# Kernel optimization log

Hardware: AMD Instinct MI355X
Metric: run time of the kernel (lower is better)

The kernel has to match this reference:

```python
import jax, jax.numpy as jnp
import numpy as np

NEG_SLOPE = 0.01  # torch F.leaky_relu default
NUM_USER, NUM_ITEM, DIM = 50000, 30000, 64
N_NODES = NUM_USER + NUM_ITEM
N_INTER = 800000
N_LAYERS = 2


def _leaky(x):
    return jax.nn.leaky_relu(x, NEG_SLOPE)


def _gcn_tower(features, preference, id_embedding, W, b, row, col):
    # x = cat(preference, features); F.normalize (L2 per row)
    x = jnp.concatenate([preference, features], axis=0)  # [N, 64]
    x = x / jnp.maximum(jnp.linalg.norm(x, axis=1, keepdims=True), 1e-12)
    deg = jax.ops.segment_sum(jnp.ones(row.shape, x.dtype), row, num_segments=N_NODES)  # bincount(row)
    for i in range(N_LAYERS):
        # Abstract_GCN: scatter-mean of gathered neighbor feats, then linear
        agg = jax.ops.segment_sum(x[col], row, num_segments=N_NODES) / deg[:, None]
        h = _leaky(agg @ W[i, 0].T + b[i, 0])
        # has_id=True, concate=False
        x_hat = _leaky(x @ W[i, 1].T + b[i, 1]) + id_embedding
        x = _leaky(h @ W[i, 2].T + b[i, 2] + x_hat)
    return x


def setup_inputs() -> dict:
    key = jax.random.key(0)
    ks = jax.random.split(key, 14)
    # bipartite user->item edges with full node coverage (every node appears
    # as a row after symmetrization, matching real interaction data where
    # bincount(row) has no zeros)
    r1 = jnp.arange(NUM_USER, dtype=jnp.int64 if jax.config.jax_enable_x64 else jnp.int32)
    c1 = jax.random.randint(ks[0], (NUM_USER,), NUM_USER, N_NODES)
    r2 = jax.random.randint(ks[1], (NUM_ITEM,), 0, NUM_USER)
    c2 = NUM_USER + jnp.arange(NUM_ITEM, dtype=r1.dtype)
    rest = N_INTER - NUM_USER - NUM_ITEM
    r3 = jax.random.randint(ks[2], (rest,), 0, NUM_USER)
    c3 = jax.random.randint(ks[3], (rest,), NUM_USER, N_NODES)
    row0 = jnp.concatenate([r1, r2, r3])
    col0 = jnp.concatenate([c1, c2, c3])
    # symmetrize: cat(edge_index, edge_index[[1,0]])
    edge_index = jnp.stack([jnp.concatenate([row0, col0]),
                            jnp.concatenate([col0, row0])])  # [2, 1.6M]
    s = 0.1  # xavier-ish scale for 64x64
    return {
        "v_feat": jax.random.normal(ks[4], (NUM_ITEM, DIM), jnp.float32),
        "t_feat": jax.random.normal(ks[5], (NUM_ITEM, DIM), jnp.float32),
        "id_embedding": jax.random.normal(ks[6], (N_NODES, DIM), jnp.float32) * s,
        "v_pref": jax.random.normal(ks[7], (NUM_USER, DIM), jnp.float32) * s,
        "t_pref": jax.random.normal(ks[8], (NUM_USER, DIM), jnp.float32) * s,
        "v_W": jax.random.normal(ks[9], (N_LAYERS, 3, DIM, DIM), jnp.float32) * s,
        "v_b": jnp.zeros((N_LAYERS, 3, DIM), jnp.float32),
        "t_W": jax.random.normal(ks[10], (N_LAYERS, 3, DIM, DIM), jnp.float32) * s,
        "t_b": jnp.zeros((N_LAYERS, 3, DIM), jnp.float32),
        "edge_index": edge_index,
    }


def reference(v_feat, t_feat, id_embedding, v_pref, t_pref, v_W, v_b, t_W, t_b, edge_index):
    row, col = edge_index[0], edge_index[1]
    rep_v = _gcn_tower(v_feat, v_pref, id_embedding, v_W, v_b, row, col)
    rep_t = _gcn_tower(t_feat, t_pref, id_embedding, t_W, t_b, row, col)
    return (rep_v + rep_t) / 2.0  # MMGCN.get_rep representation
```

## Files before the change

kernel.cpp:

```cpp
#include <hip/hip_runtime.h>
#include <hip/hip_bf16.h>

#define NUM_USER 50000
#define N_NODES  80000
#define DIM      64
#define NEG_SLOPE 0.01f

#define NB 313
#define BSHIFT 8
#define RMASK 255
#define CSHIFT 17
#define CMASK 0x1FFFF

typedef __attribute__((ext_vector_type(8))) short short8;
typedef __attribute__((ext_vector_type(4))) float f32x4;

typedef unsigned short XT;

__device__ __forceinline__ float leaky(float v) {
    return v > 0.0f ? v : v * NEG_SLOPE;
}

__device__ __forceinline__ int load_idx(const void* ei, int is64, long long pos) {
    if (is64) return (int)((const long long*)ei)[pos];
    return ((const int*)ei)[pos];
}
__device__ __forceinline__ float load_f(const void* p, int isbf16, size_t i) {
    if (isbf16) return __bfloat162float(((const __hip_bfloat16*)p)[i]);
    return ((const float*)p)[i];
}

__device__ __forceinline__ unsigned short f2bf(float f) {
    unsigned u = __float_as_uint(f);
    u += 0x7fffu + ((u >> 16) & 1u);
    return (unsigned short)(u >> 16);
}

__global__ void detect_kernel(const unsigned int* __restrict__ feat_words,
                              const int* __restrict__ ei_words,
                              int* __restrict__ flags) {
    int lane = threadIdx.x & 63;
    int orv = 0;
    for (int i = lane * 2 + 1; i < 1024; i += 128) orv |= ei_words[i];
    int hits = 0;
    for (int i = lane; i < 256; i += 64) {
        unsigned e = (feat_words[i] >> 7) & 0xFF;
        hits += (e == 126 || e == 127) ? 1 : 0;
    }
    #pragma unroll
    for (int d = 32; d > 0; d >>= 1) {
        orv  |= __shfl_xor(orv, d, 64);
        hits += __shfl_xor(hits, d, 64);
    }
    if (lane == 0 && blockIdx.x == 0) {
        flags[0] = (orv == 0) ? 1 : 0;
        flags[1] = (hits > 64) ? 1 : 0;
    }
}

__global__ __launch_bounds__(1024) void prep_kernel(
        const void* __restrict__ vW, const void* __restrict__ tW,
        const void* __restrict__ vb, const void* __restrict__ tb,
        const int* __restrict__ flags,
        int* __restrict__ bucketCnt, unsigned short* __restrict__ Wbf,
        float* __restrict__ bfp) {
    int idx = blockIdx.x * blockDim.x + threadIdx.x;
    int isb = flags[1];
    if (idx < 320) {
        bucketCnt[idx] = 0;
    } else {
        int j = idx - 320;
        if (j < 2 * 24576) {
            int tw = j / 24576, r = j % 24576;
            Wbf[j] = f2bf(load_f(tw ? tW : vW, isb, r));
        } else if (j < 2 * 24576 + 2 * 384) {
            int i2 = j - 2 * 24576;
            int tw = i2 / 384, r = i2 % 384;
            bfp[i2] = load_f(tw ? tb : vb, isb, r);
        }
    }
}

__global__ __launch_bounds__(256) void countinit_kernel(
        const void* __restrict__ ei, int E, int cntBlocks,
        const int* __restrict__ flags,
        int* __restrict__ bucketCnt,
        const void* __restrict__ vp, const void* __restrict__ tp,
        const void* __restrict__ vf, const void* __restrict__ tf,
        XT* __restrict__ xc) {
    if ((int)blockIdx.x < cntBlocks) {
        __shared__ int bcnt[320];
        int tid = threadIdx.x;
        for (int i = tid; i < 320; i += 256) bcnt[i] = 0;
        __syncthreads();
        int is64 = flags[0];
        int base = blockIdx.x * 2048;
        #pragma unroll
        for (int it = 0; it < 8; ++it) {
            int e = base + it * 256 + tid;
            if (e < E) {
                int r = load_idx(ei, is64, e);
                int c = load_idx(ei, is64, (long long)E + e);
                if ((unsigned)r < N_NODES && (unsigned)c < N_NODES)
                    atomicAdd(&bcnt[r >> BSHIFT], 1);
            }
        }
        __syncthreads();
        for (int i = tid; i < NB; i += 256) {
            int v = bcnt[i];
            if (v) atomicAdd(&bucketCnt[i], v);
        }
    } else {
        int n = (blockIdx.x - cntBlocks) * 4 + (threadIdx.x >> 6);
        if (n >= N_NODES) return;
        int lane = threadIdx.x & 63;
        int isb = flags[1];
        float a, b;
        if (n < NUM_USER) {
            a = load_f(vp, isb, (size_t)n * DIM + lane);
            b = load_f(tp, isb, (size_t)n * DIM + lane);
        } else {
            a = load_f(vf, isb, (size_t)(n - NUM_USER) * DIM + lane);
            b = load_f(tf, isb, (size_t)(n - NUM_USER) * DIM + lane);
        }
        float sa = a * a, sb = b * b;
        #pragma unroll
        for (int d = 32; d > 0; d >>= 1) {
            sa += __shfl_xor(sa, d, 64);
            sb += __shfl_xor(sb, d, 64);
        }
        float ra = 1.0f / fmaxf(sqrtf(sa), 1e-12f);
        float rb = 1.0f / fmaxf(sqrtf(sb), 1e-12f);
        xc[(size_t)n * 128 + lane]      = f2bf(a * ra);
        xc[(size_t)n * 128 + 64 + lane] = f2bf(b * rb);
    }
}

__global__ __launch_bounds__(512) void bucketscan_kernel(
        const int* __restrict__ bucketCnt,
        int* __restrict__ bucketBase, int* __restrict__ bucketCur) {
    __shared__ int sc[512];
    int t = threadIdx.x;
    int v = (t < NB) ? bucketCnt[t] : 0;
    sc[t] = v;
    __syncthreads();
    for (int d = 1; d < 512; d <<= 1) {
        int x = sc[t];
        int y = (t >= d) ? sc[t - d] : 0;
        __syncthreads();
        sc[t] = x + y;
        __syncthreads();
    }
    if (t < NB) {
        int excl = sc[t] - v;
        bucketBase[t] = excl;
        bucketCur[t]  = excl;
        if (t == NB - 1) bucketBase[NB] = sc[t];
    }
}

__global__ __launch_bounds__(320) void binplace_kernel(
        const void* __restrict__ ei, int E,
        const int* __restrict__ flags,
        int* __restrict__ bucketCur, unsigned int* __restrict__ recs) {
    __shared__ int bloc[320];
    __shared__ int bres[320];
    int tid = threadIdx.x;
    bloc[tid] = 0;
    __syncthreads();
    int is64 = flags[0];
    int base = blockIdx.x * 2560;

    int bb[8], cc[8], lp[8], rl[8];
    #pragma unroll
    for (int it = 0; it < 8; ++it) {
        bb[it] = -1;
        int e = base + it * 320 + tid;
        if (e < E) {
            int r = load_idx(ei, is64, e);
            int c = load_idx(ei, is64, (long long)E + e);
            if ((unsigned)r < N_NODES && (unsigned)c < N_NODES) {
                int b = r >> BSHIFT;
                bb[it] = b;
                cc[it] = c;
                rl[it] = r & RMASK;
                lp[it] = atomicAdd(&bloc[b], 1);
            }
        }
    }
    __syncthreads();
    if (tid < NB) {
        int v = bloc[tid];
        bres[tid] = v ? atomicAdd(&bucketCur[tid], v) : 0;
    }
    __syncthreads();
    #pragma unroll
    for (int it = 0; it < 8; ++it) {
        if (bb[it] >= 0) {
            int pos = bres[bb[it]] + lp[it];
            recs[pos] = ((unsigned)rl[it] << CSHIFT) | (unsigned)cc[it];
        }
    }
}

__global__ __launch_bounds__(512) void bin2csr_kernel(
        const unsigned int* __restrict__ recs,
        const int* __restrict__ bucketBase,
        int* __restrict__ cnt, int* __restrict__ cur,
        int* __restrict__ csr) {
    __shared__ int rcnt[256];
    __shared__ int sc[256];
    __shared__ int lcur[256];
    int b = blockIdx.x;
    int t = threadIdx.x;
    int base = bucketBase[b];
    int count = bucketBase[b + 1] - base;

    if (t < 256) { rcnt[t] = 0; lcur[t] = 0; }
    __syncthreads();
    for (int i = t; i < count; i += 512) {
        unsigned rec = recs[base + i];
        atomicAdd(&rcnt[rec >> CSHIFT], 1);
    }
    __syncthreads();
    int v = (t < 256) ? rcnt[t] : 0;
    if (t < 256) sc[t] = v;
    __syncthreads();
    for (int d = 1; d < 256; d <<= 1) {
        int x = 0;
        if (t < 256) { x = sc[t]; if (t >= d) x += sc[t - d]; }
        __syncthreads();
        if (t < 256) sc[t] = x;
        __syncthreads();
    }
    if (t < 256) {
        int row = (b << BSHIFT) + t;
        if (row < N_NODES) {
            cnt[row] = v;
            cur[row] = base + sc[t];
        }
    }
    __syncthreads();
    for (int i = t; i < count; i += 512) {
        unsigned rec = recs[base + i];
        int rloc = rec >> CSHIFT;
        int c = rec & CMASK;
        int pos = base + (sc[rloc] - rcnt[rloc]) + atomicAdd(&lcur[rloc], 1);
        csr[pos] = c;
    }
}

__global__ __launch_bounds__(512) void gather_kernel(
        const XT* __restrict__ xc, XT* __restrict__ agg,
        const int* __restrict__ cnt, const int* __restrict__ cur,
        const int* __restrict__ csr) {
    int n = blockIdx.x * 8 + (threadIdx.x >> 6);
    if (n >= N_NODES) return;
    int lane = threadIdx.x & 63;
    int g8 = lane >> 3;
    int s  = lane & 7;
    int gg = g8 >> 1;
    int h  = g8 & 1;

    int d = cnt[n];
    int base = cur[n] - d;
    const int* nb = csr + base;
    const XT* xh = xc + h * 64;

    float acc[8];
    #pragma unroll
    for (int f = 0; f < 8; ++f) acc[f] = 0.f;

    int jj = gg;
    for (; jj + 4 < d; jj += 8) {
        int c0 = nb[jj];
        int c1 = nb[jj + 4];
        uint4 r0 = ((const uint4*)(xh + (size_t)c0 * 128))[s];
        uint4 r1 = ((const uint4*)(xh + (size_t)c1 * 128))[s];
        acc[0] += __uint_as_float(r0.x << 16);
        acc[1] += __uint_as_float(r0.x & 0xffff0000u);
        acc[2] += __uint_as_float(r0.y << 16);
        acc[3] += __uint_as_float(r0.y & 0xffff0000u);
        acc[4] += __uint_as_float(r0.z << 16);
        acc[5] += __uint_as_float(r0.z & 0xffff0000u);
        acc[6] += __uint_as_float(r0.w << 16);
        acc[7] += __uint_as_float(r0.w & 0xffff0000u);
        acc[0] += __uint_as_float(r1.x << 16);
        acc[1] += __uint_as_float(r1.x & 0xffff0000u);
        acc[2] += __uint_as_float(r1.y << 16);
        acc[3] += __uint_as_float(r1.y & 0xffff0000u);
        acc[4] += __uint_as_float(r1.z << 16);
        acc[5] += __uint_as_float(r1.z & 0xffff0000u);
        acc[6] += __uint_as_float(r1.w << 16);
        acc[7] += __uint_as_float(r1.w & 0xffff0000u);
    }
    if (jj < d) {
        int c0 = nb[jj];
        uint4 r0 = ((const uint4*)(xh + (size_t)c0 * 128))[s];
        acc[0] += __uint_as_float(r0.x << 16);
        acc[1] += __uint_as_float(r0.x & 0xffff0000u);
        acc[2] += __uint_as_float(r0.y << 16);
        acc[3] += __uint_as_float(r0.y & 0xffff0000u);
        acc[4] += __uint_as_float(r0.z << 16);
        acc[5] += __uint_as_float(r0.z & 0xffff0000u);
        acc[6] += __uint_as_float(r0.w << 16);
        acc[7] += __uint_as_float(r0.w & 0xffff0000u);
    }

    #pragma unroll
    for (int dd = 16; dd < 64; dd <<= 1) {
        #pragma unroll
        for (int f = 0; f < 8; ++f) acc[f] += __shfl_xor(acc[f], dd, 64);
    }

    float invd = (d > 0) ? 1.0f / (float)d : 0.0f;
    if (g8 < 2) {
        uint4 w;
        w.x = (unsigned)f2bf(acc[0] * invd) | ((unsigned)f2bf(acc[1] * invd) << 16);
        w.y = (unsigned)f2bf(acc[2] * invd) | ((unsigned)f2bf(acc[3] * invd) << 16);
        w.z = (unsigned)f2bf(acc[4] * invd) | ((unsigned)f2bf(acc[5] * invd) << 16);
        w.w = (unsigned)f2bf(acc[6] * invd) | ((unsigned)f2bf(acc[7] * invd) << 16);
        ((uint4*)(agg + (size_t)n * 128 + h * 64))[s] = w;
    }
}

__global__ __launch_bounds__(256) void dense_mfma_kernel(
        XT* __restrict__ xc, const XT* __restrict__ agg,
        const void* __restrict__ id_emb,
        const unsigned short* __restrict__ Wbf, const float* __restrict__ bfp,
        int layer, const int* __restrict__ flags) {
    __shared__ unsigned short hts[4][16 * 72];
    int wave = threadIdx.x >> 6, lane = threadIdx.x & 63;
    int quad = lane >> 4, l16 = lane & 15;
    int tower = blockIdx.y;
    int isb = flags[1];
    int n0 = (blockIdx.x * 4 + wave) * 16;
    int toff = tower * 64;
    const unsigned short* Wm = Wbf + (size_t)((tower * 2 + layer) * 3) * 4096;
    const float* bb = bfp + (tower * 2 + layer) * 192;
    unsigned short* ht = hts[wave];

    size_t arow = (size_t)(n0 + l16) * 128 + toff + quad * 8;

    short8 a0, a1;
    f32x4 accP[4];

    a0 = *(const short8*)(xc + arow);
    a1 = *(const short8*)(xc + arow + 32);
    #pragma unroll
    for (int t = 0; t < 4; ++t) {
        f32x4 c = {0.f, 0.f, 0.f, 0.f};
        short8 b0 = *(const short8*)(Wm + 4096 + (16 * t + l16) * 64 + quad * 8);
        short8 b1 = *(const short8*)(Wm + 4096 + (16 * t + l16) * 64 + 32 + quad * 8);
        c = __builtin_amdgcn_mfma_f32_16x16x32_bf16(a0, b0, c, 0, 0, 0);
        c = __builtin_amdgcn_mfma_f32_16x16x32_bf16(a1, b1, c, 0, 0, 0);
        float bias = bb[64 + 16 * t + l16];
        #pragma unroll
        for (int r = 0; r < 4; ++r) accP[t][r] = leaky(c[r] + bias);
    }

    a0 = *(const short8*)(agg + arow);
    a1 = *(const short8*)(agg + arow + 32);
    #pragma unroll
    for (int t = 0; t < 4; ++t) {
        f32x4 c = {0.f, 0.f, 0.f, 0.f};
        short8 b0 = *(const short8*)(Wm + (16 * t + l16) * 64 + quad * 8);
        short8 b1 = *(const short8*)(Wm + (16 * t + l16) * 64 + 32 + quad * 8);
        c = __builtin_amdgcn_mfma_f32_16x16x32_bf16(a0, b0, c, 0, 0, 0);
        c = __builtin_amdgcn_mfma_f32_16x16x32_bf16(a1, b1, c, 0, 0, 0);
        float bias = bb[16 * t + l16];
        #pragma unroll
        for (int r = 0; r < 4; ++r)
            ht[(quad * 4 + r) * 72 + 16 * t + l16] = f2bf(leaky(c[r] + bias));
    }

    a0 = *(const short8*)(ht + l16 * 72 + quad * 8);
    a1 = *(const short8*)(ht + l16 * 72 + 32 + quad * 8);
    #pragma unroll
    for (int t = 0; t < 4; ++t) {
        f32x4 c = {0.f, 0.f, 0.f, 0.f};
        short8 b0 = *(const short8*)(Wm + 2 * 4096 + (16 * t + l16) * 64 + quad * 8);
        short8 b1 = *(const short8*)(Wm + 2 * 4096 + (16 * t + l16) * 64 + 32 + quad * 8);
        c = __builtin_amdgcn_mfma_f32_16x16x32_bf16(a0, b0, c, 0, 0, 0);
        c = __builtin_amdgcn_mfma_f32_16x16x32_bf16(a1, b1, c, 0, 0, 0);
        float bias = bb[128 + 16 * t + l16];
        #pragma unroll
        for (int r = 0; r < 4; ++r) {
            int node = n0 + quad * 4 + r;
            int j = 16 * t + l16;
            float idv = load_f(id_emb, isb, (size_t)node * 64 + j);
            xc[(size_t)node * 128 + toff + j] = f2bf(leaky(c[r] + bias + accP[t][r] + idv));
        }
    }
}

__global__ void final_kernel(const XT* __restrict__ xc, void* __restrict__ out,
                             const int* __restrict__ flags, int n8) {
    int i = blockIdx.x * blockDim.x + threadIdx.x;
    if (i >= n8) return;
    int n = i >> 3, s = i & 7;
    uint4 v = ((const uint4*)(xc + (size_t)n * 128))[s];
    uint4 t = ((const uint4*)(xc + (size_t)n * 128 + 64))[s];
    float r[8];
    r[0] = (__uint_as_float(v.x << 16) + __uint_as_float(t.x << 16)) * 0.5f;
    r[1] = (__uint_as_float(v.x & 0xffff0000u) + __uint_as_float(t.x & 0xffff0000u)) * 0.5f;
    r[2] = (__uint_as_float(v.y << 16) + __uint_as_float(t.y << 16)) * 0.5f;
    r[3] = (__uint_as_float(v.y & 0xffff0000u) + __uint_as_float(t.y & 0xffff0000u)) * 0.5f;
    r[4] = (__uint_as_float(v.z << 16) + __uint_as_float(t.z << 16)) * 0.5f;
    r[5] = (__uint_as_float(v.z & 0xffff0000u) + __uint_as_float(t.z & 0xffff0000u)) * 0.5f;
    r[6] = (__uint_as_float(v.w << 16) + __uint_as_float(t.w << 16)) * 0.5f;
    r[7] = (__uint_as_float(v.w & 0xffff0000u) + __uint_as_float(t.w & 0xffff0000u)) * 0.5f;
    if (flags[1]) {
        uint4 o;
        o.x = (unsigned)f2bf(r[0]) | ((unsigned)f2bf(r[1]) << 16);
        o.y = (unsigned)f2bf(r[2]) | ((unsigned)f2bf(r[3]) << 16);
        o.z = (unsigned)f2bf(r[4]) | ((unsigned)f2bf(r[5]) << 16);
        o.w = (unsigned)f2bf(r[6]) | ((unsigned)f2bf(r[7]) << 16);
        ((uint4*)out)[i] = o;
    } else {
        float4* o = (float4*)out;
        o[i * 2 + 0] = make_float4(r[0], r[1], r[2], r[3]);
        o[i * 2 + 1] = make_float4(r[4], r[5], r[6], r[7]);
    }
}

extern "C" void kernel_launch(void* const* d_in, const int* in_sizes, int n_in,
                              void* d_out, int out_size, void* d_ws, size_t ws_size,
                              hipStream_t stream) {
    const void* v_feat = d_in[0];
    const void* t_feat = d_in[1];
    const void* id_emb = d_in[2];
    const void* v_pref = d_in[3];
    const void* t_pref = d_in[4];
    const void* v_W    = d_in[5];
    const void* v_b    = d_in[6];
    const void* t_W    = d_in[7];
    const void* t_b    = d_in[8];
    const void* ei     = d_in[9];

    const int E = in_sizes[9] / 2;
    char* ws = (char*)d_ws;

    size_t o = 0;
    int*            flags     = (int*)(ws + o);            o += 16;
    int*            cnt       = (int*)(ws + o);            o += 320000;
    int*            cur       = (int*)(ws + o);            o += 320000;
    int*            bucketCnt = (int*)(ws + o);            o += 320 * 4;
    int*            bucketBase= (int*)(ws + o);            o += 320 * 4;
    int*            bucketCur = (int*)(ws + o);            o += 320 * 4;
    unsigned short* Wbf       = (unsigned short*)(ws + o); o += 2 * 24576 * 2;
    float*          bfp       = (float*)(ws + o);          o += 2 * 384 * 4;
    XT* xc  = (XT*)(ws + o); o += (size_t)N_NODES * 128 * sizeof(XT);
    XT* agg = (XT*)(ws + o); o += (size_t)N_NODES * 128 * sizeof(XT);
    unsigned int* recs = (unsigned int*)(ws + o); o += (size_t)E * 4;
    int* csr = (int*)(ws + o);

    detect_kernel<<<dim3(1), dim3(64), 0, stream>>>(
        (const unsigned int*)v_feat, (const int*)ei, flags);

    prep_kernel<<<dim3((320 + 2 * 24576 + 2 * 384 + 1023) / 1024), dim3(1024), 0, stream>>>(
        v_W, t_W, v_b, t_b, flags, bucketCnt, Wbf, bfp);

    const int cntBlocks  = (E + 2047) / 2048;
    const int initBlocks = (N_NODES + 3) / 4;
    countinit_kernel<<<dim3(cntBlocks + initBlocks), dim3(256), 0, stream>>>(
        ei, E, cntBlocks, flags, bucketCnt,
        v_pref, t_pref, v_feat, t_feat, xc);

    bucketscan_kernel<<<dim3(1), dim3(512), 0, stream>>>(bucketCnt, bucketBase, bucketCur);

    binplace_kernel<<<dim3((E + 2559) / 2560), dim3(320), 0, stream>>>(
        ei, E, flags, bucketCur, recs);

    bin2csr_kernel<<<dim3(NB), dim3(512), 0, stream>>>(recs, bucketBase, cnt, cur, csr);

    const int gatherBlocks = (N_NODES + 7) / 8;
    const int denseBlocks  = N_NODES / (16 * 4);

    for (int layer = 0; layer < 2; ++layer) {
        gather_kernel<<<dim3(gatherBlocks), dim3(512), 0, stream>>>(xc, agg, cnt, cur, csr);
        dense_mfma_kernel<<<dim3(denseBlocks, 2), dim3(256), 0, stream>>>(
            xc, agg, id_emb, Wbf, bfp, layer, flags);
    }

    const int n8 = N_NODES * DIM / 8;
    final_kernel<<<dim3((n8 + 255) / 256), dim3(256), 0, stream>>>(xc, d_out, flags, n8);
}
```

Measured before the change: 416.2 us.

## Fuse neighbor gather into dense MFMA kernel with ping-pong feature buffers

The separate gather kernel is removed. Each dense MFMA kernel now computes its node's neighbor mean directly into bf16 A-fragments, which avoids writing and re-reading the intermediate agg buffer and drops two launches. Layers alternate between two feature buffers so reads and writes never alias. The weight/bias packing is folded into the countinit launch and the bucket-count zeroing into detect, removing the prep kernel. The trade-off is that each wave now walks the neighbors of 16 nodes with 4 lanes per node. This gives fewer waves in flight, less coalesced row reads, and divergence from uneven degrees within a wave.

```diff
diff --git a/kernel.cpp b/kernel.cpp
--- a/kernel.cpp
+++ b/kernel.cpp
@@ -36,10 +36,23 @@
     return (unsigned short)(u >> 16);
 }
 
+__device__ __forceinline__ void acc8(float* a, uint4 r) {
+    a[0] += __uint_as_float(r.x << 16);
+    a[1] += __uint_as_float(r.x & 0xffff0000u);
+    a[2] += __uint_as_float(r.y << 16);
+    a[3] += __uint_as_float(r.y & 0xffff0000u);
+    a[4] += __uint_as_float(r.z << 16);
+    a[5] += __uint_as_float(r.z & 0xffff0000u);
+    a[6] += __uint_as_float(r.w << 16);
+    a[7] += __uint_as_float(r.w & 0xffff0000u);
+}
+
 __global__ void detect_kernel(const unsigned int* __restrict__ feat_words,
                               const int* __restrict__ ei_words,
-                              int* __restrict__ flags) {
+                              int* __restrict__ flags,
+                              int* __restrict__ bucketCnt) {
     int lane = threadIdx.x & 63;
+    for (int i = lane; i < 320; i += 64) bucketCnt[i] = 0;
     int orv = 0;
     for (int i = lane * 2 + 1; i < 1024; i += 128) orv |= ei_words[i];
     int hits = 0;
@@ -58,36 +71,16 @@
     }
 }
 
-__global__ __launch_bounds__(1024) void prep_kernel(
-        const void* __restrict__ vW, const void* __restrict__ tW,
-        const void* __restrict__ vb, const void* __restrict__ tb,
-        const int* __restrict__ flags,
-        int* __restrict__ bucketCnt, unsigned short* __restrict__ Wbf,
-        float* __restrict__ bfp) {
-    int idx = blockIdx.x * blockDim.x + threadIdx.x;
-    int isb = flags[1];
-    if (idx < 320) {
-        bucketCnt[idx] = 0;
-    } else {
-        int j = idx - 320;
-        if (j < 2 * 24576) {
-            int tw = j / 24576, r = j % 24576;
-            Wbf[j] = f2bf(load_f(tw ? tW : vW, isb, r));
-        } else if (j < 2 * 24576 + 2 * 384) {
-            int i2 = j - 2 * 24576;
-            int tw = i2 / 384, r = i2 % 384;
-            bfp[i2] = load_f(tw ? tb : vb, isb, r);
-        }
-    }
-}
-
 __global__ __launch_bounds__(256) void countinit_kernel(
-        const void* __restrict__ ei, int E, int cntBlocks,
+        const void* __restrict__ ei, int E, int cntBlocks, int initBlocks,
         const int* __restrict__ flags,
         int* __restrict__ bucketCnt,
         const void* __restrict__ vp, const void* __restrict__ tp,
         const void* __restrict__ vf, const void* __restrict__ tf,
-        XT* __restrict__ xc) {
+        XT* __restrict__ xc,
+        const void* __restrict__ vW, const void* __restrict__ tW,
+        const void* __restrict__ vb, const void* __restrict__ tb,
+        unsigned short* __restrict__ Wbf, float* __restrict__ bfp) {
     if ((int)blockIdx.x < cntBlocks) {
         __shared__ int bcnt[320];
         int tid = threadIdx.x;
@@ -110,7 +103,7 @@
             int v = bcnt[i];
             if (v) atomicAdd(&bucketCnt[i], v);
         }
-    } else {
+    } else if ((int)blockIdx.x < cntBlocks + initBlocks) {
         int n = (blockIdx.x - cntBlocks) * 4 + (threadIdx.x >> 6);
         if (n >= N_NODES) return;
         int lane = threadIdx.x & 63;
@@ -133,6 +126,17 @@
         float rb = 1.0f / fmaxf(sqrtf(sb), 1e-12f);
         xc[(size_t)n * 128 + lane]      = f2bf(a * ra);
         xc[(size_t)n * 128 + 64 + lane] = f2bf(b * rb);
+    } else {
+        int isb = flags[1];
+        int j = (blockIdx.x - cntBlocks - initBlocks) * 256 + threadIdx.x;
+        if (j < 2 * 24576) {
+            int tw = j / 24576, r = j % 24576;
+            Wbf[j] = f2bf(load_f(tw ? tW : vW, isb, r));
+        } else if (j < 2 * 24576 + 2 * 384) {
+            int i2 = j - 2 * 24576;
+            int tw = i2 / 384, r = i2 % 384;
+            bfp[i2] = load_f(tw ? tb : vb, isb, r);
+        }
     }
 }
 
@@ -250,84 +254,12 @@
     }
 }
 
-__global__ __launch_bounds__(512) void gather_kernel(
-        const XT* __restrict__ xc, XT* __restrict__ agg,
-        const int* __restrict__ cnt, const int* __restrict__ cur,
-        const int* __restrict__ csr) {
-    int n = blockIdx.x * 8 + (threadIdx.x >> 6);
-    if (n >= N_NODES) return;
-    int lane = threadIdx.x & 63;
-    int g8 = lane >> 3;
-    int s  = lane & 7;
-    int gg = g8 >> 1;
-    int h  = g8 & 1;
-
-    int d = cnt[n];
-    int base = cur[n] - d;
-    const int* nb = csr + base;
-    const XT* xh = xc + h * 64;
-
-    float acc[8];
-    #pragma unroll
-    for (int f = 0; f < 8; ++f) acc[f] = 0.f;
-
-    int jj = gg;
-    for (; jj + 4 < d; jj += 8) {
-        int c0 = nb[jj];
-        int c1 = nb[jj + 4];
-        uint4 r0 = ((const uint4*)(xh + (size_t)c0 * 128))[s];
-        uint4 r1 = ((const uint4*)(xh + (size_t)c1 * 128))[s];
-        acc[0] += __uint_as_float(r0.x << 16);
-        acc[1] += __uint_as_float(r0.x & 0xffff0000u);
-        acc[2] += __uint_as_float(r0.y << 16);
-        acc[3] += __uint_as_float(r0.y & 0xffff0000u);
-        acc[4] += __uint_as_float(r0.z << 16);
-        acc[5] += __uint_as_float(r0.z & 0xffff0000u);
-        acc[6] += __uint_as_float(r0.w << 16);
-        acc[7] += __uint_as_float(r0.w & 0xffff0000u);
-        acc[0] += __uint_as_float(r1.x << 16);
-        acc[1] += __uint_as_float(r1.x & 0xffff0000u);
-        acc[2] += __uint_as_float(r1.y << 16);
-        acc[3] += __uint_as_float(r1.y & 0xffff0000u);
-        acc[4] += __uint_as_float(r1.z << 16);
-        acc[5] += __uint_as_float(r1.z & 0xffff0000u);
-        acc[6] += __uint_as_float(r1.w << 16);
-        acc[7] += __uint_as_float(r1.w & 0xffff0000u);
-    }
-    if (jj < d) {
-        int c0 = nb[jj];
-        uint4 r0 = ((const uint4*)(xh + (size_t)c0 * 128))[s];
-        acc[0] += __uint_as_float(r0.x << 16);
-        acc[1] += __uint_as_float(r0.x & 0xffff0000u);
-        acc[2] += __uint_as_float(r0.y << 16);
-        acc[3] += __uint_as_float(r0.y & 0xffff0000u);
-        acc[4] += __uint_as_float(r0.z << 16);
-        acc[5] += __uint_as_float(r0.z & 0xffff0000u);
-        acc[6] += __uint_as_float(r0.w << 16);
-        acc[7] += __uint_as_float(r0.w & 0xffff0000u);
-    }
-
-    #pragma unroll
-    for (int dd = 16; dd < 64; dd <<= 1) {
-        #pragma unroll
-        for (int f = 0; f < 8; ++f) acc[f] += __shfl_xor(acc[f], dd, 64);
-    }
-
-    float invd = (d > 0) ? 1.0f / (float)d : 0.0f;
-    if (g8 < 2) {
-        uint4 w;
-        w.x = (unsigned)f2bf(acc[0] * invd) | ((unsigned)f2bf(acc[1] * invd) << 16);
-        w.y = (unsigned)f2bf(acc[2] * invd) | ((unsigned)f2bf(acc[3] * invd) << 16);
-        w.z = (unsigned)f2bf(acc[4] * invd) | ((unsigned)f2bf(acc[5] * invd) << 16);
-        w.w = (unsigned)f2bf(acc[6] * invd) | ((unsigned)f2bf(acc[7] * invd) << 16);
-        ((uint4*)(agg + (size_t)n * 128 + h * 64))[s] = w;
-    }
-}
-
-__global__ __launch_bounds__(256) void dense_mfma_kernel(
-        XT* __restrict__ xc, const XT* __restrict__ agg,
+__global__ __launch_bounds__(256) void dense_fused_kernel(
+        const XT* __restrict__ xin, XT* __restrict__ xout,
         const void* __restrict__ id_emb,
         const unsigned short* __restrict__ Wbf, const float* __restrict__ bfp,
+        const int* __restrict__ cnt, const int* __restrict__ cur,
+        const int* __restrict__ csr,
         int layer, const int* __restrict__ flags) {
     __shared__ unsigned short hts[4][16 * 72];
     int wave = threadIdx.x >> 6, lane = threadIdx.x & 63;
@@ -340,13 +272,51 @@
     const float* bb = bfp + (tower * 2 + layer) * 192;
     unsigned short* ht = hts[wave];
 
+    int node = n0 + l16;
+    int d = cnt[node];
+    int base = cur[node] - d;
+    const int* nb = csr + base;
+    const XT* xt = xin + toff + quad * 8;
+
+    float g0[8], g1[8];
+    #pragma unroll
+    for (int f = 0; f < 8; ++f) { g0[f] = 0.f; g1[f] = 0.f; }
+
+    int jj = 0;
+    for (; jj + 1 < d; jj += 2) {
+        int c0 = nb[jj];
+        int c1 = nb[jj + 1];
+        const XT* p0 = xt + (size_t)c0 * 128;
+        const XT* p1 = xt + (size_t)c1 * 128;
+        uint4 u0 = *(const uint4*)(p0);
+        uint4 w0 = *(const uint4*)(p0 + 32);
+        uint4 u1 = *(const uint4*)(p1);
+        uint4 w1 = *(const uint4*)(p1 + 32);
+        acc8(g0, u0); acc8(g1, w0);
+        acc8(g0, u1); acc8(g1, w1);
+    }
+    if (jj < d) {
+        int c0 = nb[jj];
+        const XT* p0 = xt + (size_t)c0 * 128;
+        uint4 u0 = *(const uint4*)(p0);
+        uint4 w0 = *(const uint4*)(p0 + 32);
+        acc8(g0, u0); acc8(g1, w0);
+    }
+    float invd = (d > 0) ? 1.0f / (float)d : 0.0f;
+    short8 ga0, ga1;
+    #pragma unroll
+    for (int f = 0; f < 8; ++f) {
+        ga0[f] = (short)f2bf(g0[f] * invd);
+        ga1[f] = (short)f2bf(g1[f] * invd);
+    }
+
     size_t arow = (size_t)(n0 + l16) * 128 + toff + quad * 8;
 
     short8 a0, a1;
     f32x4 accP[4];
 
-    a0 = *(const short8*)(xc + arow);
-    a1 = *(const short8*)(xc + arow + 32);
+    a0 = *(const short8*)(xin + arow);
+    a1 = *(const short8*)(xin + arow + 32);
     #pragma unroll
     for (int t = 0; t < 4; ++t) {
         f32x4 c = {0.f, 0.f, 0.f, 0.f};
@@ -359,15 +329,13 @@
         for (int r = 0; r < 4; ++r) accP[t][r] = leaky(c[r] + bias);
     }
 
-    a0 = *(const short8*)(agg + arow);
-    a1 = *(const short8*)(agg + arow + 32);
     #pragma unroll
     for (int t = 0; t < 4; ++t) {
         f32x4 c = {0.f, 0.f, 0.f, 0.f};
         short8 b0 = *(const short8*)(Wm + (16 * t + l16) * 64 + quad * 8);
         short8 b1 = *(const short8*)(Wm + (16 * t + l16) * 64 + 32 + quad * 8);
-        c = __builtin_amdgcn_mfma_f32_16x16x32_bf16(a0, b0, c, 0, 0, 0);
-        c = __builtin_amdgcn_mfma_f32_16x16x32_bf16(a1, b1, c, 0, 0, 0);
+        c = __builtin_amdgcn_mfma_f32_16x16x32_bf16(ga0, b0, c, 0, 0, 0);
+        c = __builtin_amdgcn_mfma_f32_16x16x32_bf16(ga1, b1, c, 0, 0, 0);
         float bias = bb[16 * t + l16];
         #pragma unroll
         for (int r = 0; r < 4; ++r)
@@ -386,10 +354,10 @@
         float bias = bb[128 + 16 * t + l16];
         #pragma unroll
         for (int r = 0; r < 4; ++r) {
-            int node = n0 + quad * 4 + r;
+            int node2 = n0 + quad * 4 + r;
             int j = 16 * t + l16;
-            float idv = load_f(id_emb, isb, (size_t)node * 64 + j);
-            xc[(size_t)node * 128 + toff + j] = f2bf(leaky(c[r] + bias + accP[t][r] + idv));
+            float idv = load_f(id_emb, isb, (size_t)node2 * 64 + j);
+            xout[(size_t)node2 * 128 + toff + j] = f2bf(leaky(c[r] + bias + accP[t][r] + idv));
         }
     }
 }
@@ -450,22 +418,21 @@
     int*            bucketCur = (int*)(ws + o);            o += 320 * 4;
     unsigned short* Wbf       = (unsigned short*)(ws + o); o += 2 * 24576 * 2;
     float*          bfp       = (float*)(ws + o);          o += 2 * 384 * 4;
-    XT* xc  = (XT*)(ws + o); o += (size_t)N_NODES * 128 * sizeof(XT);
-    XT* agg = (XT*)(ws + o); o += (size_t)N_NODES * 128 * sizeof(XT);
+    XT* xcA = (XT*)(ws + o); o += (size_t)N_NODES * 128 * sizeof(XT);
+    XT* xcB = (XT*)(ws + o); o += (size_t)N_NODES * 128 * sizeof(XT);
     unsigned int* recs = (unsigned int*)(ws + o); o += (size_t)E * 4;
     int* csr = (int*)(ws + o);
 
     detect_kernel<<<dim3(1), dim3(64), 0, stream>>>(
-        (const unsigned int*)v_feat, (const int*)ei, flags);
-
-    prep_kernel<<<dim3((320 + 2 * 24576 + 2 * 384 + 1023) / 1024), dim3(1024), 0, stream>>>(
-        v_W, t_W, v_b, t_b, flags, bucketCnt, Wbf, bfp);
+        (const unsigned int*)v_feat, (const int*)ei, flags, bucketCnt);
 
     const int cntBlocks  = (E + 2047) / 2048;
     const int initBlocks = (N_NODES + 3) / 4;
-    countinit_kernel<<<dim3(cntBlocks + initBlocks), dim3(256), 0, stream>>>(
-        ei, E, cntBlocks, flags, bucketCnt,
-        v_pref, t_pref, v_feat, t_feat, xc);
+    const int packBlocks = (2 * 24576 + 2 * 384 + 255) / 256;
+    countinit_kernel<<<dim3(cntBlocks + initBlocks + packBlocks), dim3(256), 0, stream>>>(
+        ei, E, cntBlocks, initBlocks, flags, bucketCnt,
+        v_pref, t_pref, v_feat, t_feat, xcA,
+        v_W, t_W, v_b, t_b, Wbf, bfp);
 
     bucketscan_kernel<<<dim3(1), dim3(512), 0, stream>>>(bucketCnt, bucketBase, bucketCur);
 
@@ -474,15 +441,13 @@
 
     bin2csr_kernel<<<dim3(NB), dim3(512), 0, stream>>>(recs, bucketBase, cnt, cur, csr);
 
-    const int gatherBlocks = (N_NODES + 7) / 8;
-    const int denseBlocks  = N_NODES / (16 * 4);
-
-    for (int layer = 0; layer < 2; ++layer) {
-        gather_kernel<<<dim3(gatherBlocks), dim3(512), 0, stream>>>(xc, agg, cnt, cur, csr);
-        dense_mfma_kernel<<<dim3(denseBlocks, 2), dim3(256), 0, stream>>>(
-            xc, agg, id_emb, Wbf, bfp, layer, flags);
-    }
+    const int denseBlocks = N_NODES / (16 * 4);
+
+    dense_fused_kernel<<<dim3(denseBlocks, 2), dim3(256), 0, stream>>>(
+        xcA, xcB, id_emb, Wbf, bfp, cnt, cur, csr, 0, flags);
+    dense_fused_kernel<<<dim3(denseBlocks, 2), dim3(256), 0, stream>>>(
+        xcB, xcA, id_emb, Wbf, bfp, cnt, cur, csr, 1, flags);
 
     const int n8 = N_NODES * DIM / 8;
-    final_kernel<<<dim3((n8 + 255) / 256), dim3(256), 0, stream>>>(xc, d_out, flags, n8);
-}
+    final_kernel<<<dim3((n8 + 255) / 256), dim3(256), 0, stream>>>(xcA, d_out, flags, n8);
+}
```

After: 472.9 us. 13.6% more time.
